# Optimization experiments

Hardware: AMD Instinct MI355X
Metric: run time of the kernel (lower is better)

## Reference

```python
import jax, jax.numpy as jnp
import numpy as np


def setup_inputs() -> dict:
    key = jax.random.key(0)
    # [batch, seq, 2*d_ff]; first half is gate, second half is up projection output
    x = jax.random.normal(key, (4, 2048, 32768), dtype=jnp.float32)
    return {"x": x}


def reference(x) -> jnp.ndarray:
    # SiluAndMul.forward_native: chunk last dim in two, silu(gate) * up
    d = x.shape[-1] // 2
    gate = x[..., :d]
    up = x[..., d:]
    return jax.nn.silu(gate) * up
```

## Files before the change

### kernel.cpp

```cpp
#include <hip/hip_runtime.h>
#include <hip/hip_bf16.h>


#define D4_HALF  4096
#define D4_FULL  8192
#define BLOCK    256
#define GRID     512
#define ITER     256

typedef float f4 __attribute__((ext_vector_type(4)));

__device__ __forceinline__ float silu(float x) {
    return x * __builtin_amdgcn_rcpf(1.0f + expf(-x));
}

__device__ __forceinline__ f4 silu_mul(f4 g, f4 u) {
    f4 r;
    r.x = silu(g.x) * u.x;
    r.y = silu(g.y) * u.y;
    r.z = silu(g.z) * u.z;
    r.w = silu(g.w) * u.w;
    return r;
}

__global__ void __launch_bounds__(BLOCK)
SiluAndMul_kernel(const f4* __restrict__ x, f4* __restrict__ out) {
    long long base = (long long)blockIdx.x * (BLOCK * ITER) + threadIdx.x;
#pragma unroll 2
    for (int j = 0; j < ITER; j += 2) {
        long long i0 = base + (long long)j * BLOCK;
        long long i1 = i0 + BLOCK;
        long long r0 = i0 >> 12, c0 = i0 & (D4_HALF - 1);
        long long r1 = i1 >> 12, c1 = i1 & (D4_HALF - 1);
        long long gi0 = r0 * D4_FULL + c0;
        long long gi1 = r1 * D4_FULL + c1;
        f4 g0 = x[gi0];
        f4 u0 = x[gi0 + D4_HALF];
        f4 g1 = x[gi1];
        f4 u1 = x[gi1 + D4_HALF];
        out[i0] = silu_mul(g0, u0);
        out[i1] = silu_mul(g1, u1);
    }
}

extern "C" void kernel_launch(void* const* d_in, const int* in_sizes, int n_in,
                              void* d_out, int out_size, void* d_ws, size_t ws_size,
                              hipStream_t stream) {
    const f4* x = (const f4*)d_in[0];
    f4* out = (f4*)d_out;
    SiluAndMul_kernel<<<GRID, BLOCK, 0, stream>>>(x, out);
}
```

Before: 307.1 us.

## Software-pipeline loads in batches of four with double buffering and 32-bit indexing

Restructures the streaming loop so each thread loads a batch of four gate/up vector pairs ahead while it computes and stores the previous batch, using two register buffers. Index arithmetic also moves from 64-bit to 32-bit ints, which cuts address computation. The goal is more memory-level parallelism per thread to hide HBM latency. The costs are higher register pressure and reliance on the total element count fitting in 32-bit indexes (16M f4 elements, which it does).

Measured after the change: 294.8 us. 4.0% less time.

```diff
diff --git a/kernel.cpp b/kernel.cpp
--- a/kernel.cpp
+++ b/kernel.cpp
@@ -7,6 +7,8 @@
 #define BLOCK    256
 #define GRID     512
 #define ITER     256
+#define BATCH    4
+#define NBATCH   (ITER / BATCH)
 
 typedef float f4 __attribute__((ext_vector_type(4)));
 
@@ -14,32 +16,44 @@
     return x * __builtin_amdgcn_rcpf(1.0f + expf(-x));
 }
 
-__device__ __forceinline__ f4 silu_mul(f4 g, f4 u) {
-    f4 r;
-    r.x = silu(g.x) * u.x;
-    r.y = silu(g.y) * u.y;
-    r.z = silu(g.z) * u.z;
-    r.w = silu(g.w) * u.w;
+struct Batch { f4 g[BATCH]; f4 u[BATCH]; };
+
+__device__ __forceinline__ Batch load_batch(const f4* __restrict__ x,
+                                            int base, int b) {
+    Batch r;
+#pragma unroll
+    for (int k = 0; k < BATCH; ++k) {
+        int i = base + (b * BATCH + k) * BLOCK;
+        int gi = (i >> 12) * D4_FULL + (i & (D4_HALF - 1));
+        r.g[k] = x[gi];
+        r.u[k] = x[gi + D4_HALF];
+    }
     return r;
+}
+
+__device__ __forceinline__ void store_batch(f4* __restrict__ out,
+                                            int base, int b, const Batch& t) {
+#pragma unroll
+    for (int k = 0; k < BATCH; ++k) {
+        f4 r;
+        r.x = silu(t.g[k].x) * t.u[k].x;
+        r.y = silu(t.g[k].y) * t.u[k].y;
+        r.z = silu(t.g[k].z) * t.u[k].z;
+        r.w = silu(t.g[k].w) * t.u[k].w;
+        out[base + (b * BATCH + k) * BLOCK] = r;
+    }
 }
 
 __global__ void __launch_bounds__(BLOCK)
 SiluAndMul_kernel(const f4* __restrict__ x, f4* __restrict__ out) {
-    long long base = (long long)blockIdx.x * (BLOCK * ITER) + threadIdx.x;
-#pragma unroll 2
-    for (int j = 0; j < ITER; j += 2) {
-        long long i0 = base + (long long)j * BLOCK;
-        long long i1 = i0 + BLOCK;
-        long long r0 = i0 >> 12, c0 = i0 & (D4_HALF - 1);
-        long long r1 = i1 >> 12, c1 = i1 & (D4_HALF - 1);
-        long long gi0 = r0 * D4_FULL + c0;
-        long long gi1 = r1 * D4_FULL + c1;
-        f4 g0 = x[gi0];
-        f4 u0 = x[gi0 + D4_HALF];
-        f4 g1 = x[gi1];
-        f4 u1 = x[gi1 + D4_HALF];
-        out[i0] = silu_mul(g0, u0);
-        out[i1] = silu_mul(g1, u1);
+    int base = blockIdx.x * (BLOCK * ITER) + threadIdx.x;
+    Batch A = load_batch(x, base, 0);
+#pragma unroll 1
+    for (int b = 0; b < NBATCH; b += 2) {
+        Batch B = load_batch(x, base, b + 1);
+        store_batch(out, base, b, A);
+        if (b + 2 < NBATCH) A = load_batch(x, base, b + 2);
+        store_batch(out, base, b + 1, B);
     }
 }
 
```
